# Kernel optimization log

Measured on AMD Instinct MI355X. Metric: run time of the kernel, lower is better.

Reference implementation:

```python
import jax, jax.numpy as jnp
import numpy as np

N_HEADS = 8
EPS = 1e-5


def setup_inputs() -> dict:
    key = jax.random.key(0)
    ks = jax.random.split(key, 5)
    c = 512
    x = jax.random.normal(ks[0], (2, c, 2, 32, 32), dtype=jnp.float32)
    s = 0.02
    Wq = jax.random.normal(ks[1], (c, c), dtype=jnp.float32) * s
    Wk = jax.random.normal(ks[2], (c, c), dtype=jnp.float32) * s
    Wv = jax.random.normal(ks[3], (c, c), dtype=jnp.float32) * s
    Wo = jax.random.normal(ks[4], (c, c), dtype=jnp.float32) * s
    bo = jnp.zeros((c,), dtype=jnp.float32)
    gamma = jnp.ones((c,), dtype=jnp.float32)
    beta = jnp.zeros((c,), dtype=jnp.float32)
    return {"x": x, "Wq": Wq, "Wk": Wk, "Wv": Wv, "Wo": Wo, "bo": bo,
            "gamma": gamma, "beta": beta}


def reference(x, Wq, Wk, Wv, Wo, bo, gamma, beta):
    b, c, d, h, w = x.shape
    seq = d * h * w
    # [b, c, d, h, w] -> [b, seq, c]
    xs = jnp.transpose(x, (0, 2, 3, 4, 1)).reshape(b, seq, c)
    # LayerNorm over channel dim
    mu = jnp.mean(xs, axis=-1, keepdims=True)
    var = jnp.mean(jnp.square(xs - mu), axis=-1, keepdims=True)
    xn = (xs - mu) * jax.lax.rsqrt(var + EPS) * gamma + beta
    # Self-attention (cond falls back to x); weights stored [in, out]
    dh = c // N_HEADS
    q = (xn @ Wq).reshape(b, seq, N_HEADS, dh)
    k = (xn @ Wk).reshape(b, seq, N_HEADS, dh)
    v = (xn @ Wv).reshape(b, seq, N_HEADS, dh)
    scale = dh ** (-0.5)
    attn = jnp.einsum('bihd,bjhd->bhij', q, k) * scale  # [b, H, seq, seq]
    attn = jax.nn.softmax(attn, axis=-1)
    out = jnp.einsum('bhij,bjhd->bihd', attn, v).reshape(b, seq, c)
    out = out @ Wo + bo
    y = out + xs  # residual
    return jnp.transpose(y.reshape(b, d, h, w, c), (0, 4, 1, 2, 3))
```

## Files before the change

kernel.cpp:

```cpp
#include <hip/hip_runtime.h>
#include <cstdint>

typedef unsigned short u16;
typedef unsigned char u8;
typedef __bf16 bf16x8 __attribute__((ext_vector_type(8)));
typedef float f32x4 __attribute__((ext_vector_type(4)));
typedef u16 u16x4 __attribute__((ext_vector_type(4)));
typedef u16 u16x8 __attribute__((ext_vector_type(8)));
typedef long l64x2 __attribute__((ext_vector_type(2)));

__device__ __forceinline__ u16 f2bf(float f) {
  union { float f; unsigned u; } v; v.f = f;
  unsigned r = v.u + 0x7FFFu + ((v.u >> 16) & 1u);
  return (u16)(r >> 16);
}

__device__ __forceinline__ float bf2f(u16 u) {
  union { unsigned u; float f; } c; c.u = ((unsigned)u) << 16;
  return c.f;
}

__device__ __forceinline__ f32x4 mfma16(bf16x8 a, bf16x8 b, f32x4 c) {
  return __builtin_amdgcn_mfma_f32_16x16x32_bf16(a, b, c, 0, 0, 0);
}

__device__ __forceinline__ f32x4 mfma8(long a, long b, f32x4 c) {
  return __builtin_amdgcn_mfma_f32_16x16x32_fp8_fp8(a, b, c, 0, 0, 0);
}

__device__ __forceinline__ u8 f2fp8(float f) {
  return (u8)(__builtin_amdgcn_cvt_pk_fp8_f32(f, f, 0, false) & 0xff);
}

__device__ __forceinline__ void gload_lds16(const void* g, void* l) {
  auto* lp = reinterpret_cast<__attribute__((address_space(3))) unsigned int*>(
      reinterpret_cast<uintptr_t>(l));
  const auto* gp = reinterpret_cast<const __attribute__((address_space(1))) unsigned int*>(
      reinterpret_cast<uintptr_t>(g));
  __builtin_amdgcn_global_load_lds(gp, lp, 16, 0, 0);
}

template <int N>
__device__ __forceinline__ void waitcnt_vm() {
  if constexpr (N == 0)      asm volatile("s_waitcnt vmcnt(0)" ::: "memory");
  else if constexpr (N == 2) asm volatile("s_waitcnt vmcnt(2)" ::: "memory");
  else if constexpr (N == 4) asm volatile("s_waitcnt vmcnt(4)" ::: "memory");
  else if constexpr (N == 6) asm volatile("s_waitcnt vmcnt(6)" ::: "memory");
  else                       asm volatile("s_waitcnt vmcnt(8)" ::: "memory");
}

__global__ __launch_bounds__(256) void prep_kernel(const float* __restrict__ Wq,
                                                   const float* __restrict__ Wk,
                                                   const float* __restrict__ Wv,
                                                   const float* __restrict__ Wo,
                                                   const float* __restrict__ x,
                                                   const float* __restrict__ gamma,
                                                   const float* __restrict__ beta,
                                                   u16* __restrict__ wt_out,
                                                   u16* __restrict__ xn) {
  struct LnSh {
    float red0[16][16];
    float red1[16][16];
    float mu[16], rs[16];
    u16 tile[16][520];
  };
  struct WtSh { float tile[32][33]; };
  __shared__ __align__(16) char shraw[sizeof(LnSh) > sizeof(WtSh) ? sizeof(LnSh) : sizeof(WtSh)];
  int bid = blockIdx.x;
  int t = threadIdx.x;
  if (bid < 256) {
    LnSh& S = *reinterpret_cast<LnSh*>(shraw);
    int b = bid >> 7;
    int s0 = (bid & 127) * 16;
    int tx = t & 15, ty = t >> 4;
    const float* xb = x + (size_t)b * 512 * 2048 + s0 + tx;
    float vals[32];
    float sum = 0.f, sq = 0.f;
#pragma unroll
    for (int k = 0; k < 32; k++) {
      float v = xb[(size_t)(ty + k * 16) * 2048];
      vals[k] = v;
      sum += v; sq += v * v;
    }
    S.red0[ty][tx] = sum; S.red1[ty][tx] = sq;
    __syncthreads();
    if (t < 16) {
      float a = 0.f, c2 = 0.f;
#pragma unroll
      for (int i = 0; i < 16; i++) { a += S.red0[i][t]; c2 += S.red1[i][t]; }
      float mu = a * (1.f / 512.f);
      float var = c2 * (1.f / 512.f) - mu * mu;
      S.mu[t] = mu;
      S.rs[t] = rsqrtf(var + 1e-5f);
    }
    __syncthreads();
    float mu = S.mu[tx], rs = S.rs[tx];
#pragma unroll
    for (int k = 0; k < 32; k++) {
      int ch = ty + k * 16;
      S.tile[tx][ch] = f2bf((vals[k] - mu) * rs * gamma[ch] + beta[ch]);
    }
    __syncthreads();
    int col = (t & 63) * 8;
    int r0 = t >> 6;
    u16* outb = xn + (size_t)(b * 2048 + s0) * 512;
#pragma unroll
    for (int i = 0; i < 4; i++) {
      int row = r0 + 4 * i;
      *(u16x8*)(outb + (size_t)row * 512 + col) = *(const u16x8*)(&S.tile[row][col]);
    }
  } else {
    WtSh& S = *reinterpret_cast<WtSh*>(shraw);
    int wid = bid - 256;
    int z = wid >> 8;
    const float* W = (z == 0) ? Wq : (z == 1) ? Wk : (z == 2) ? Wv : Wo;
    u16* o = wt_out + (size_t)z * 262144;
    int rem = wid & 255;
    int n0 = (rem >> 4) * 32, k0 = (rem & 15) * 32;
    int tx = t & 31, ty = t >> 5;
#pragma unroll
    for (int i = 0; i < 4; i++)
      S.tile[ty + i * 8][tx] = W[(size_t)(k0 + ty + i * 8) * 512 + n0 + tx];
    __syncthreads();
#pragma unroll
    for (int i = 0; i < 4; i++) {
      int n = ty + i * 8;
      o[(size_t)(n0 + n) * 512 + k0 + tx] = f2bf(S.tile[tx][n]);
    }
  }
}

template <int AM, int AN>
__device__ __forceinline__ void gemm_tile_ring(const u16* __restrict__ A, const u16* __restrict__ B,
                                               int m0, int n0, f32x4 acc[AM][AN],
                                               u16* As, u16* Bs) {
  constexpr int BM = AM * 32, BN = AN * 32;
  constexpr int LA = BM / 64, LB = BN / 64;
  constexpr int L = LA + LB;
  int t = threadIdx.x;
  int w = t >> 6, lane = t & 63;
  int wm = w >> 1, wn = w & 1;
  int arow = t >> 2;
  int acol = (t & 3) * 8;
  int lrow = lane & 15;
  int lko = (lane >> 4) * 8;

  auto stage = [&](int buf, int k0) {
#pragma unroll
    for (int g = 0; g < LA; ++g)
      gload_lds16(A + (size_t)(m0 + g * 64 + arow) * 512 + k0 + acol,
                  As + buf * (BM * 32) + g * 2048 + w * 512);
#pragma unroll
    for (int g = 0; g < LB; ++g)
      gload_lds16(B + (size_t)(n0 + g * 64 + arow) * 512 + k0 + acol,
                  Bs + buf * (BN * 32) + g * 2048 + w * 512);
  };

  stage(0, 0);
  stage(1, 32);
  stage(2, 64);
  __syncthreads();

  for (int tt = 0; tt < 16; ++tt) {
    int pk = (tt + 3 < 16) ? (tt + 3) * 32 : 0;
    stage((tt + 3) & 3, pk);
    const u16* as = As + (tt & 3) * (BM * 32);
    const u16* bs = Bs + (tt & 3) * (BN * 32);
    bf16x8 af[AM], bfr[AN];
#pragma unroll
    for (int i = 0; i < AM; i++) af[i] = *(const bf16x8*)(as + (wm * (AM * 16) + i * 16 + lrow) * 32 + lko);
#pragma unroll
    for (int j = 0; j < AN; j++) bfr[j] = *(const bf16x8*)(bs + (wn * (AN * 16) + j * 16 + lrow) * 32 + lko);
    __builtin_amdgcn_s_setprio(1);
#pragma unroll
    for (int i = 0; i < AM; i++)
#pragma unroll
      for (int j = 0; j < AN; j++)
        acc[i][j] = mfma16(af[i], bfr[j], acc[i][j]);
    __builtin_amdgcn_s_setprio(0);
    waitcnt_vm<2 * L>();
    __builtin_amdgcn_s_barrier();
  }
  waitcnt_vm<0>();
}

__global__ __launch_bounds__(256) void gemm_qkv(const u16* __restrict__ xn, const u16* __restrict__ wt,
                                                u8* __restrict__ Qb, u8* __restrict__ Kp,
                                                u8* __restrict__ Vp) {
  __shared__ u16 As[4 * 64 * 32];
  __shared__ u16 Bs[4 * 128 * 32];
  const float SCQ = 0.125f * 1.4426950408889634f;
  int mat = blockIdx.z;
  const u16* WT = wt + (size_t)mat * 262144;
  int m0 = blockIdx.x * 64, n0 = blockIdx.y * 128;
  f32x4 acc[2][4] = {};
  gemm_tile_ring<2, 4>(xn, WT, m0, n0, acc, As, Bs);
  int t = threadIdx.x, w = t >> 6, lane = t & 63;
  int wm = w >> 1, wn = w & 1, lrow = lane & 15, lgrp = lane >> 4;
#pragma unroll
  for (int i = 0; i < 2; i++) {
#pragma unroll
    for (int j = 0; j < 4; j++) {
      int gr0 = m0 + wm * 32 + i * 16 + lgrp * 4;
      int gc = n0 + wn * 64 + j * 16 + lrow;
      if (mat == 0) {
#pragma unroll
        for (int r = 0; r < 4; r++)
          Qb[(size_t)(gr0 + r) * 512 + gc] = f2fp8(acc[i][j][r] * SCQ);
      } else if (mat == 1) {
        int h = gc >> 6, d = gc & 63;
        int half = d >> 5, lg = (d >> 3) & 3, jj = d & 7;
#pragma unroll
        for (int r = 0; r < 4; r++) {
          int kg = gr0 + r;
          int bq = kg >> 11, kl = kg & 2047;
          int kt = kl >> 5, kw = kl & 31;
          int tt = (kw >> 2) & 1;
          int kwb = kw - 4 * tt;
          int lr = ((kwb >> 3) << 2) | (kwb & 3);
          size_t idx = (size_t)((bq * 8 + h) * 64 + kt) * 2048 + tt * 1024 +
                       (lg * 16 + lr) * 16 + half * 8 + jj;
          Kp[idx] = f2fp8(acc[i][j][r]);
        }
      } else {
        int h = gc >> 6, d = gc & 63;
        int dt = d >> 4, lr = d & 15;
        int kg = gr0;
        int bq = kg >> 11, kl = kg & 2047;
        int kt = kl >> 5, kw = kl & 31;
        int lg = kw >> 3, j0 = kw & 7;
        unsigned u = __builtin_amdgcn_cvt_pk_fp8_f32(acc[i][j][0], acc[i][j][1], 0, false);
        u = __builtin_amdgcn_cvt_pk_fp8_f32(acc[i][j][2], acc[i][j][3], u, true);
        size_t idx = (size_t)((bq * 8 + h) * 64 + kt) * 2048 + (dt >> 1) * 1024 +
                     (lg * 16 + lr) * 16 + (dt & 1) * 8 + j0;
        *(unsigned*)(Vp + idx) = u;
      }
    }
  }
}

__global__ __launch_bounds__(256, 4) void attn_kernel(const u8* __restrict__ Qb, const u8* __restrict__ Kp,
                                                      const u8* __restrict__ Vp, u16* __restrict__ Opart,
                                                      float* __restrict__ ml, int logS) {
  const long ONES8 = 0x3838383838383838L;
  int S = 1 << logS;
  int bid = blockIdx.x;
  int qt = bid >> (4 + logS);
  int group = bid & (16 * S - 1);
  int hb = group >> logS, sp = group & (S - 1);
  int b = hb >> 3, h = hb & 7;
  int kt0 = sp * (64 >> logS);
  int nsteps = 64 >> logS;

  int t = threadIdx.x, w = t >> 6, lane = t & 63;
  int lrow = lane & 15, lgrp = lane >> 4, lko = lgrp * 8;
  int q0 = qt * 128 + w * 32;

  const u8* Qp = Qb + (size_t)(b * 2048 + q0 + lrow) * 512 + h * 64 + lko;
  long qa0 = *(const long*)(Qp);
  long qa1 = *(const long*)(Qp + 32);
  long qb0 = *(const long*)(Qp + 16 * 512);
  long qb1 = *(const long*)(Qp + 16 * 512 + 32);

  const u8* Kbh = Kp + (size_t)hb * 131072 + lane * 16;
  const u8* Vbh = Vp + (size_t)hb * 131072 + lane * 16;

  f32x4 acca[4] = {}, accb[4] = {};
  f32x4 suma = {}, sumb = {};

  long kA[4], vA[4], kB[4], vB[4];

  auto loadKV = [&](long* kf, long* vf, int st) {
    const u8* pk = Kbh + (size_t)(kt0 + st) * 2048;
    const u8* pv = Vbh + (size_t)(kt0 + st) * 2048;
    l64x2 a0 = *(const l64x2*)(pk);
    l64x2 a1 = *(const l64x2*)(pk + 1024);
    l64x2 b0 = *(const l64x2*)(pv);
    l64x2 b1 = *(const l64x2*)(pv + 1024);
    kf[0] = a0[0]; kf[1] = a0[1]; kf[2] = a1[0]; kf[3] = a1[1];
    vf[0] = b0[0]; vf[1] = b0[1]; vf[2] = b1[0]; vf[3] = b1[1];
  };

  auto computeStep = [&](const long* kc, const long* vc) {
    f32x4 sa0 = {}, sa1 = {}, sb0 = {}, sb1 = {};
    __builtin_amdgcn_s_setprio(1);
    sa0 = mfma8(kc[0], qa0, sa0);
    sa0 = mfma8(kc[1], qa1, sa0);
    sa1 = mfma8(kc[2], qa0, sa1);
    sa1 = mfma8(kc[3], qa1, sa1);
    sb0 = mfma8(kc[0], qb0, sb0);
    sb0 = mfma8(kc[1], qb1, sb0);
    sb1 = mfma8(kc[2], qb0, sb1);
    sb1 = mfma8(kc[3], qb1, sb1);
    __builtin_amdgcn_s_setprio(0);

    float pa[8], pb8[8];
#pragma unroll
    for (int jj = 0; jj < 4; jj++) pa[jj] = exp2f(sa0[jj]);
#pragma unroll
    for (int jj = 0; jj < 4; jj++) pa[4 + jj] = exp2f(sa1[jj]);
#pragma unroll
    for (int jj = 0; jj < 4; jj++) pb8[jj] = exp2f(sb0[jj]);
#pragma unroll
    for (int jj = 0; jj < 4; jj++) pb8[4 + jj] = exp2f(sb1[jj]);

    unsigned alo = __builtin_amdgcn_cvt_pk_fp8_f32(pa[0], pa[1], 0, false);
    alo = __builtin_amdgcn_cvt_pk_fp8_f32(pa[2], pa[3], alo, true);
    unsigned ahi = __builtin_amdgcn_cvt_pk_fp8_f32(pa[4], pa[5], 0, false);
    ahi = __builtin_amdgcn_cvt_pk_fp8_f32(pa[6], pa[7], ahi, true);
    long pla = (long)(((unsigned long long)ahi << 32) | alo);
    unsigned blo = __builtin_amdgcn_cvt_pk_fp8_f32(pb8[0], pb8[1], 0, false);
    blo = __builtin_amdgcn_cvt_pk_fp8_f32(pb8[2], pb8[3], blo, true);
    unsigned bhi = __builtin_amdgcn_cvt_pk_fp8_f32(pb8[4], pb8[5], 0, false);
    bhi = __builtin_amdgcn_cvt_pk_fp8_f32(pb8[6], pb8[7], bhi, true);
    long plb = (long)(((unsigned long long)bhi << 32) | blo);

    __builtin_amdgcn_s_setprio(1);
    acca[0] = mfma8(pla, vc[0], acca[0]);
    acca[1] = mfma8(pla, vc[1], acca[1]);
    acca[2] = mfma8(pla, vc[2], acca[2]);
    acca[3] = mfma8(pla, vc[3], acca[3]);
    accb[0] = mfma8(plb, vc[0], accb[0]);
    accb[1] = mfma8(plb, vc[1], accb[1]);
    accb[2] = mfma8(plb, vc[2], accb[2]);
    accb[3] = mfma8(plb, vc[3], accb[3]);
    suma = mfma8(pla, ONES8, suma);
    sumb = mfma8(plb, ONES8, sumb);
    __builtin_amdgcn_s_setprio(0);
  };

  loadKV(kA, vA, 0);
  for (int st = 0; st < nsteps; st += 2) {
    loadKV(kB, vB, (st + 1 < nsteps) ? st + 1 : 0);
    computeStep(kA, vA);
    loadKV(kA, vA, (st + 2 < nsteps) ? st + 2 : 0);
    computeStep(kB, vB);
  }

  if (lrow == 0) {
    int rowa = b * 2048 + q0 + lgrp * 4;
#pragma unroll
    for (int r = 0; r < 4; r++) {
      ml[(size_t)sp * 32768 + (rowa + r) * 8 + h] = suma[r];
      ml[(size_t)sp * 32768 + (rowa + 16 + r) * 8 + h] = sumb[r];
    }
  }

  u16* Ao = Opart + (size_t)sp * 2097152 + (size_t)(b * 2048 + q0) * 512 + h * 64;
#pragma unroll
  for (int r = 0; r < 4; r++) {
#pragma unroll
    for (int dt = 0; dt < 4; dt++) {
      Ao[(size_t)(lgrp * 4 + r) * 512 + dt * 16 + lrow] = f2bf(acca[dt][r]);
      Ao[(size_t)(16 + lgrp * 4 + r) * 512 + dt * 16 + lrow] = f2bf(accb[dt][r]);
    }
  }
}

template <int S>
__global__ __launch_bounds__(256) void attn_combine(const u16* __restrict__ Opart,
                                                    const float* __restrict__ ml,
                                                    u16* __restrict__ AO) {
  int gid = blockIdx.x * 256 + threadIdx.x;
  int pair = gid >> 3, dcol = (gid & 7) * 8;
  int row = pair >> 3, h = pair & 7;
  float lsum = 0.f;
#pragma unroll
  for (int s = 0; s < S; s++) lsum += ml[(size_t)s * 32768 + pair];
  float inv = 1.0f / lsum;
  float o[8] = {};
#pragma unroll
  for (int s = 0; s < S; s++) {
    u16x8 ov = *(const u16x8*)(Opart + (size_t)s * 2097152 + (size_t)row * 512 + h * 64 + dcol);
#pragma unroll
    for (int j = 0; j < 8; j++) o[j] += bf2f(ov[j]);
  }
  u16x8 outv;
#pragma unroll
  for (int j = 0; j < 8; j++) outv[j] = f2bf(o[j] * inv);
  *(u16x8*)(AO + (size_t)row * 512 + h * 64 + dcol) = outv;
}

__global__ __launch_bounds__(256) void gemm_out(const u16* __restrict__ AO, const u16* __restrict__ WoT,
                                                const float* __restrict__ bo, const float* __restrict__ x,
                                                float* __restrict__ y) {
  __shared__ u16 As[4 * 64 * 32];
  __shared__ u16 Bs[4 * 64 * 32];
  int m0 = blockIdx.x * 64, n0 = blockIdx.y * 64;
  f32x4 acc[2][2] = {};
  gemm_tile_ring<2, 2>(AO, WoT, m0, n0, acc, As, Bs);
  int t = threadIdx.x, w = t >> 6, lane = t & 63;
  int wm = w >> 1, wn = w & 1, lrow = lane & 15, lgrp = lane >> 4;
#pragma unroll
  for (int i = 0; i < 2; i++) {
#pragma unroll
    for (int j = 0; j < 2; j++) {
      int gr0 = m0 + wm * 32 + i * 16 + lgrp * 4;
      int gc = n0 + wn * 32 + j * 16 + lrow;
      int bb = gr0 >> 11, s = gr0 & 2047;
      float bias = bo[gc];
      const float* xp = x + ((size_t)bb * 512 + gc) * 2048 + s;
      float4 xv = *(const float4*)xp;
      float4 o;
      o.x = acc[i][j][0] + bias + xv.x;
      o.y = acc[i][j][1] + bias + xv.y;
      o.z = acc[i][j][2] + bias + xv.z;
      o.w = acc[i][j][3] + bias + xv.w;
      *(float4*)(y + ((size_t)bb * 512 + gc) * 2048 + s) = o;
    }
  }
}

extern "C" void kernel_launch(void* const* d_in, const int* in_sizes, int n_in,
                              void* d_out, int out_size, void* d_ws, size_t ws_size,
                              hipStream_t stream) {
  const float* x = (const float*)d_in[0];
  const float* Wq = (const float*)d_in[1];
  const float* Wk = (const float*)d_in[2];
  const float* Wv = (const float*)d_in[3];
  const float* Wo = (const float*)d_in[4];
  const float* bo = (const float*)d_in[5];
  const float* gamma = (const float*)d_in[6];
  const float* beta = (const float*)d_in[7];
  float* y = (float*)d_out;
  char* ws = (char*)d_ws;
  u16* xn = (u16*)(ws);
  u16* wt = (u16*)(ws + (4 << 20));
  u8* Qb = (u8*)(ws + (6 << 20));
  u8* Kp = (u8*)(ws + (10 << 20));
  u8* Vp = (u8*)(ws + (14 << 20));
  u16* AO = (u16*)(ws + (18 << 20));
  float* ml = (float*)(ws + (22 << 20));
  u16* Opart = (u16*)(ws + (23 << 20));

  int logS;
  if (ws_size >= (40u << 20)) logS = 2;
  else if (ws_size >= (32u << 20)) logS = 1;
  else { logS = 0; Opart = AO; }

  prep_kernel<<<dim3(1280), dim3(256), 0, stream>>>(Wq, Wk, Wv, Wo, x, gamma, beta, wt, xn);
  gemm_qkv<<<dim3(64, 4, 3), dim3(256), 0, stream>>>(xn, wt, Qb, Kp, Vp);
  attn_kernel<<<dim3(256 << logS), dim3(256), 0, stream>>>(Qb, Kp, Vp, Opart, ml, logS);
  if (logS == 2)      attn_combine<4><<<dim3(1024), dim3(256), 0, stream>>>(Opart, ml, AO);
  else if (logS == 1) attn_combine<2><<<dim3(1024), dim3(256), 0, stream>>>(Opart, ml, AO);
  else                attn_combine<1><<<dim3(1024), dim3(256), 0, stream>>>(Opart, ml, AO);
  gemm_out<<<dim3(64, 8), dim3(256), 0, stream>>>(AO, wt + 3 * 262144, bo, x, y);
}
```

Before: 63.86 us.

## Quantize QKV GEMM inputs to fp8 in fragment-packed layout, drop LDS staging

Result: faster. 57.57 us (-9.9%).

```diff
diff --git a/kernel.cpp b/kernel.cpp
--- a/kernel.cpp
+++ b/kernel.cpp
@@ -1,5 +1,6 @@
 #include <hip/hip_runtime.h>
 #include <cstdint>
+#include <cstring>
 
 typedef unsigned short u16;
 typedef unsigned char u8;
@@ -56,13 +57,14 @@
                                                    const float* __restrict__ x,
                                                    const float* __restrict__ gamma,
                                                    const float* __restrict__ beta,
-                                                   u16* __restrict__ wt_out,
-                                                   u16* __restrict__ xn) {
+                                                   u8* __restrict__ wt8f,
+                                                   u16* __restrict__ wtWo,
+                                                   u8* __restrict__ xn8f) {
   struct LnSh {
     float red0[16][16];
     float red1[16][16];
     float mu[16], rs[16];
-    u16 tile[16][520];
+    u8 tile8[16][520];
   };
   struct WtSh { float tile[32][33]; };
   __shared__ __align__(16) char shraw[sizeof(LnSh) > sizeof(WtSh) ? sizeof(LnSh) : sizeof(WtSh)];
@@ -98,23 +100,25 @@
 #pragma unroll
     for (int k = 0; k < 32; k++) {
       int ch = ty + k * 16;
-      S.tile[tx][ch] = f2bf((vals[k] - mu) * rs * gamma[ch] + beta[ch]);
+      S.tile8[tx][ch] = f2fp8((vals[k] - mu) * rs * gamma[ch] + beta[ch]);
     }
     __syncthreads();
-    int col = (t & 63) * 8;
-    int r0 = t >> 6;
-    u16* outb = xn + (size_t)(b * 2048 + s0) * 512;
-#pragma unroll
-    for (int i = 0; i < 4; i++) {
-      int row = r0 + 4 * i;
-      *(u16x8*)(outb + (size_t)row * 512 + col) = *(const u16x8*)(&S.tile[row][col]);
+    int lrow2 = t & 15, kt = t >> 4;
+    int grow = b * 2048 + s0;
+    int rt2 = grow >> 5;
+    int ihalf = (s0 >> 4) & 1;
+    u8* dst = xn8f + ((size_t)rt2 * 16 + kt) * 1024 + ihalf * 8;
+#pragma unroll
+    for (int kg = 0; kg < 4; kg++) {
+      unsigned long long v;
+      memcpy(&v, &S.tile8[lrow2][kt * 32 + kg * 8], 8);
+      *(unsigned long long*)(dst + (size_t)(lrow2 + kg * 16) * 16) = v;
     }
   } else {
     WtSh& S = *reinterpret_cast<WtSh*>(shraw);
     int wid = bid - 256;
     int z = wid >> 8;
     const float* W = (z == 0) ? Wq : (z == 1) ? Wk : (z == 2) ? Wv : Wo;
-    u16* o = wt_out + (size_t)z * 262144;
     int rem = wid & 255;
     int n0 = (rem >> 4) * 32, k0 = (rem & 15) * 32;
     int tx = t & 31, ty = t >> 5;
@@ -122,10 +126,26 @@
     for (int i = 0; i < 4; i++)
       S.tile[ty + i * 8][tx] = W[(size_t)(k0 + ty + i * 8) * 512 + n0 + tx];
     __syncthreads();
-#pragma unroll
-    for (int i = 0; i < 4; i++) {
-      int n = ty + i * 8;
-      o[(size_t)(n0 + n) * 512 + k0 + tx] = f2bf(S.tile[tx][n]);
+    if (z < 3) {
+      if (t < 128) {
+        int lane = t >> 1, jhalf = t & 1;
+        int nn = (lane & 15) + jhalf * 16;
+        int kk0 = (lane >> 4) * 8;
+        u8 pk[8];
+#pragma unroll
+        for (int j = 0; j < 8; j++) pk[j] = f2fp8(S.tile[kk0 + j][nn]);
+        unsigned long long v;
+        memcpy(&v, pk, 8);
+        size_t addr = (size_t)z * 262144 + ((size_t)(n0 >> 5) * 16 + (k0 >> 5)) * 1024 +
+                      (size_t)lane * 16 + jhalf * 8;
+        *(unsigned long long*)(wt8f + addr) = v;
+      }
+    } else {
+#pragma unroll
+      for (int i = 0; i < 4; i++) {
+        int n = ty + i * 8;
+        wtWo[(size_t)(n0 + n) * 512 + k0 + tx] = f2bf(S.tile[tx][n]);
+      }
     }
   }
 }
@@ -184,25 +204,52 @@
   waitcnt_vm<0>();
 }
 
-__global__ __launch_bounds__(256) void gemm_qkv(const u16* __restrict__ xn, const u16* __restrict__ wt,
-                                                u8* __restrict__ Qb, u8* __restrict__ Kp,
-                                                u8* __restrict__ Vp) {
-  __shared__ u16 As[4 * 64 * 32];
-  __shared__ u16 Bs[4 * 128 * 32];
+__global__ __launch_bounds__(256, 4) void gemm_qkv(const u8* __restrict__ xn8f, const u8* __restrict__ wt8f,
+                                                   u8* __restrict__ Qb, u8* __restrict__ Kp,
+                                                   u8* __restrict__ Vp) {
   const float SCQ = 0.125f * 1.4426950408889634f;
   int mat = blockIdx.z;
-  const u16* WT = wt + (size_t)mat * 262144;
-  int m0 = blockIdx.x * 64, n0 = blockIdx.y * 128;
+  int bx = blockIdx.x, by = blockIdx.y;
+  int t = threadIdx.x, w = t >> 6, lane = t & 63;
+  int lrow = lane & 15, lgrp = lane >> 4;
+
+  const u8* Af = xn8f + (size_t)(bx * 4 + w) * 16384 + (size_t)lane * 16;
+  const u8* Bf = wt8f + (size_t)mat * 262144 + (size_t)(by * 2) * 16384 + (size_t)lane * 16;
+
   f32x4 acc[2][4] = {};
-  gemm_tile_ring<2, 4>(xn, WT, m0, n0, acc, As, Bs);
-  int t = threadIdx.x, w = t >> 6, lane = t & 63;
-  int wm = w >> 1, wn = w & 1, lrow = lane & 15, lgrp = lane >> 4;
+  long aA[2], bA[4], aB[2], bB[4];
+
+  auto loadAB = [&](long* a, long* bb, int kt) {
+    l64x2 av = *(const l64x2*)(Af + kt * 1024);
+    l64x2 b0 = *(const l64x2*)(Bf + kt * 1024);
+    l64x2 b1 = *(const l64x2*)(Bf + 16384 + kt * 1024);
+    a[0] = av[0]; a[1] = av[1];
+    bb[0] = b0[0]; bb[1] = b0[1]; bb[2] = b1[0]; bb[3] = b1[1];
+  };
+  auto step = [&](const long* a, const long* bb) {
+    __builtin_amdgcn_s_setprio(1);
+#pragma unroll
+    for (int i = 0; i < 2; i++)
+#pragma unroll
+      for (int j = 0; j < 4; j++)
+        acc[i][j] = mfma8(a[i], bb[j], acc[i][j]);
+    __builtin_amdgcn_s_setprio(0);
+  };
+
+  loadAB(aA, bA, 0);
+  for (int kt = 0; kt < 16; kt += 2) {
+    loadAB(aB, bB, (kt + 1) & 15);
+    step(aA, bA);
+    loadAB(aA, bA, (kt + 2) & 15);
+    step(aB, bB);
+  }
+
 #pragma unroll
   for (int i = 0; i < 2; i++) {
 #pragma unroll
     for (int j = 0; j < 4; j++) {
-      int gr0 = m0 + wm * 32 + i * 16 + lgrp * 4;
-      int gc = n0 + wn * 64 + j * 16 + lrow;
+      int gr0 = bx * 128 + w * 32 + i * 16 + lgrp * 4;
+      int gc = by * 64 + j * 16 + lrow;
       if (mat == 0) {
 #pragma unroll
         for (int r = 0; r < 4; r++)
@@ -214,11 +261,11 @@
         for (int r = 0; r < 4; r++) {
           int kg = gr0 + r;
           int bq = kg >> 11, kl = kg & 2047;
-          int kt = kl >> 5, kw = kl & 31;
+          int kt2 = kl >> 5, kw = kl & 31;
           int tt = (kw >> 2) & 1;
           int kwb = kw - 4 * tt;
           int lr = ((kwb >> 3) << 2) | (kwb & 3);
-          size_t idx = (size_t)((bq * 8 + h) * 64 + kt) * 2048 + tt * 1024 +
+          size_t idx = (size_t)((bq * 8 + h) * 64 + kt2) * 2048 + tt * 1024 +
                        (lg * 16 + lr) * 16 + half * 8 + jj;
           Kp[idx] = f2fp8(acc[i][j][r]);
         }
@@ -227,11 +274,11 @@
         int dt = d >> 4, lr = d & 15;
         int kg = gr0;
         int bq = kg >> 11, kl = kg & 2047;
-        int kt = kl >> 5, kw = kl & 31;
+        int kt2 = kl >> 5, kw = kl & 31;
         int lg = kw >> 3, j0 = kw & 7;
         unsigned u = __builtin_amdgcn_cvt_pk_fp8_f32(acc[i][j][0], acc[i][j][1], 0, false);
         u = __builtin_amdgcn_cvt_pk_fp8_f32(acc[i][j][2], acc[i][j][3], u, true);
-        size_t idx = (size_t)((bq * 8 + h) * 64 + kt) * 2048 + (dt >> 1) * 1024 +
+        size_t idx = (size_t)((bq * 8 + h) * 64 + kt2) * 2048 + (dt >> 1) * 1024 +
                      (lg * 16 + lr) * 16 + (dt & 1) * 8 + j0;
         *(unsigned*)(Vp + idx) = u;
       }
@@ -424,25 +471,26 @@
   const float* beta = (const float*)d_in[7];
   float* y = (float*)d_out;
   char* ws = (char*)d_ws;
-  u16* xn = (u16*)(ws);
-  u16* wt = (u16*)(ws + (4 << 20));
-  u8* Qb = (u8*)(ws + (6 << 20));
-  u8* Kp = (u8*)(ws + (10 << 20));
-  u8* Vp = (u8*)(ws + (14 << 20));
-  u16* AO = (u16*)(ws + (18 << 20));
-  float* ml = (float*)(ws + (22 << 20));
-  u16* Opart = (u16*)(ws + (23 << 20));
+  u8* xn8f = (u8*)(ws);
+  u8* wt8f = (u8*)(ws + (2 << 20));
+  u16* wtWo = (u16*)(ws + (3 << 20));
+  u8* Qb = (u8*)(ws + (4 << 20));
+  u8* Kp = (u8*)(ws + (6 << 20));
+  u8* Vp = (u8*)(ws + (8 << 20));
+  u16* AO = (u16*)(ws + (10 << 20));
+  float* ml = (float*)(ws + (14 << 20));
+  u16* Opart = (u16*)(ws + (15 << 20));
 
   int logS;
   if (ws_size >= (40u << 20)) logS = 2;
   else if (ws_size >= (32u << 20)) logS = 1;
   else { logS = 0; Opart = AO; }
 
-  prep_kernel<<<dim3(1280), dim3(256), 0, stream>>>(Wq, Wk, Wv, Wo, x, gamma, beta, wt, xn);
-  gemm_qkv<<<dim3(64, 4, 3), dim3(256), 0, stream>>>(xn, wt, Qb, Kp, Vp);
+  prep_kernel<<<dim3(1280), dim3(256), 0, stream>>>(Wq, Wk, Wv, Wo, x, gamma, beta, wt8f, wtWo, xn8f);
+  gemm_qkv<<<dim3(32, 8, 3), dim3(256), 0, stream>>>(xn8f, wt8f, Qb, Kp, Vp);
   attn_kernel<<<dim3(256 << logS), dim3(256), 0, stream>>>(Qb, Kp, Vp, Opart, ml, logS);
   if (logS == 2)      attn_combine<4><<<dim3(1024), dim3(256), 0, stream>>>(Opart, ml, AO);
   else if (logS == 1) attn_combine<2><<<dim3(1024), dim3(256), 0, stream>>>(Opart, ml, AO);
   else                attn_combine<1><<<dim3(1024), dim3(256), 0, stream>>>(Opart, ml, AO);
-  gemm_out<<<dim3(64, 8), dim3(256), 0, stream>>>(AO, wt + 3 * 262144, bo, x, y);
-}
+  gemm_out<<<dim3(64, 8), dim3(256), 0, stream>>>(AO, wtWo, bo, x, y);
+}
```
